# Performance work log

Measured on AMD Instinct MI355X. Metric: run time of the kernel, lower is better.

Reference implementation:

```python
import jax, jax.numpy as jnp
import numpy as np

N_NODES = 50000
N_EDGES = 1_600_000


def add_self_loops(edge_index, n):
    loops = jnp.arange(n, dtype=edge_index.dtype)
    return jnp.concatenate([edge_index, jnp.stack([loops, loops])], axis=1)


def gat_layer(x, edge_index, W, a_src, a_dst, b):
    """PyG GATConv (concat=True, negative_slope=0.2, add_self_loops handled by caller)."""
    src, dst = edge_index[0], edge_index[1]
    n = x.shape[0]
    H, C = a_src.shape
    xp = (x @ W).reshape(n, H, C)                       # [N,H,C] transformed features
    al_src = jnp.einsum('nhc,hc->nh', xp, a_src)        # [N,H]
    al_dst = jnp.einsum('nhc,hc->nh', xp, a_dst)        # [N,H]
    logits = jax.nn.leaky_relu(al_src[src] + al_dst[dst], negative_slope=0.2)  # [E,H]
    m = jax.lax.stop_gradient(jax.ops.segment_max(logits, dst, num_segments=n))
    e = jnp.exp(logits - m[dst])                        # stable segment softmax
    denom = jax.ops.segment_sum(e, dst, num_segments=n)
    alpha = e / denom[dst]                              # [E,H]
    out = jax.ops.segment_sum(xp[src] * alpha[:, :, None], dst, num_segments=n)  # [N,H,C]
    return out.reshape(n, H * C) + b


def setup_inputs() -> dict:
    key = jax.random.key(0)
    ks = jax.random.split(key, 11)
    s = 0.1  # weight scale
    return {
        'x': jax.random.normal(ks[0], (N_NODES, 128), jnp.float32),
        'edge_index': jax.random.randint(ks[1], (2, N_EDGES), 0, N_NODES, jnp.int32),
        'W1': s * jax.random.normal(ks[2], (128, 128), jnp.float32),
        'a_src1': s * jax.random.normal(ks[3], (2, 64), jnp.float32),
        'a_dst1': s * jax.random.normal(ks[4], (2, 64), jnp.float32),
        'b1': s * jax.random.normal(ks[5], (128,), jnp.float32),
        'W2': s * jax.random.normal(ks[6], (128, 64), jnp.float32),
        'a_src2': s * jax.random.normal(ks[7], (2, 32), jnp.float32),
        'a_dst2': s * jax.random.normal(ks[8], (2, 32), jnp.float32),
        'b2': s * jax.random.normal(ks[9], (64,), jnp.float32),
    }


def reference(x, edge_index, W1, a_src1, a_dst1, b1, W2, a_src2, a_dst2, b2):
    ei = add_self_loops(edge_index, x.shape[0])
    encoded = x  # FeatureEncoding with no auxiliary features: identity passthrough
    h = jax.nn.elu(gat_layer(encoded, ei, W1, a_src1, a_dst1, b1))
    out = jax.nn.elu(gat_layer(h, ei, W2, a_src2, a_dst2, b2))
    return (out, encoded)
```

## Files before the change

kernel.cpp:

```cpp
#include <hip/hip_runtime.h>
#include <math.h>

#define N_NODES 50000
#define N_EDGES 1600000
#define EA (N_EDGES + N_NODES)
#define MAXD 128
#define NBUCK 196
#define EPB 4096
#define BCAP 16000

typedef unsigned int uint32;
typedef float f32x4 __attribute__((ext_vector_type(4)));
typedef short s16x8 __attribute__((ext_vector_type(8)));

__device__ inline ushort f2bf(float f) {
  uint32 u = __float_as_uint(f);
  u += 0x7fffu + ((u >> 16) & 1u);
  return (ushort)(u >> 16);
}
__device__ inline float blo(uint32 v) { return __uint_as_float(v << 16); }
__device__ inline float bhi(uint32 v) { return __uint_as_float(v & 0xffff0000u); }
__device__ inline uint32 pack2bf(float a, float b) {
  return (uint32)f2bf(a) | ((uint32)f2bf(b) << 16);
}
__device__ inline int clampi(int v, int lo, int hi) {
  return v < lo ? lo : (v > hi ? hi : v);
}

template<int N, bool ABF>
__global__ __launch_bounds__(256) void gemm_mfma_kernel(
    const void* __restrict__ Ap, const float* __restrict__ B,
    const float* __restrict__ asrc, const float* __restrict__ adst,
    ushort* __restrict__ Cb, float* __restrict__ al, int M) {
  constexpr int KK = 4;
  constexpr int NC = N / 16;
  __shared__ uint32 Bl[KK * NC * 64 * 4];
  const int t = threadIdx.x;

  for (int id = t; id < KK * NC * 64; id += 256) {
    int lane = id & 63;
    int cf = (id >> 6) % NC;
    int kk = (id >> 6) / NC;
    int col = cf * 16 + (lane & 15);
    int k0 = kk * 32 + (lane >> 4) * 8;
    uint32 w0 = pack2bf(B[(k0 + 0) * N + col], B[(k0 + 1) * N + col]);
    uint32 w1 = pack2bf(B[(k0 + 2) * N + col], B[(k0 + 3) * N + col]);
    uint32 w2 = pack2bf(B[(k0 + 4) * N + col], B[(k0 + 5) * N + col]);
    uint32 w3 = pack2bf(B[(k0 + 6) * N + col], B[(k0 + 7) * N + col]);
    *reinterpret_cast<uint4*>(&Bl[id * 4]) = make_uint4(w0, w1, w2, w3);
  }
  __syncthreads();

  const int w = t >> 6, lane = t & 63;
  const int l15 = lane & 15, g4 = lane >> 4;
  const int row0 = blockIdx.x * 64 + w * 16;
  int arow = row0 + l15; if (arow > M - 1) arow = M - 1;
  const int k0 = g4 * 8;

  f32x4 acc[NC];
#pragma unroll
  for (int c = 0; c < NC; ++c) acc[c] = f32x4{0.f, 0.f, 0.f, 0.f};

#pragma unroll
  for (int kk = 0; kk < KK; ++kk) {
    s16x8 af;
    if (ABF) {
      af = *reinterpret_cast<const s16x8*>((const ushort*)Ap + (size_t)arow * 128 + kk * 32 + k0);
    } else {
      const float* A = (const float*)Ap;
      float4 a0 = *reinterpret_cast<const float4*>(A + (size_t)arow * 128 + kk * 32 + k0);
      float4 a1 = *reinterpret_cast<const float4*>(A + (size_t)arow * 128 + kk * 32 + k0 + 4);
      union { uint32 u[4]; s16x8 v; } p;
      p.u[0] = pack2bf(a0.x, a0.y);
      p.u[1] = pack2bf(a0.z, a0.w);
      p.u[2] = pack2bf(a1.x, a1.y);
      p.u[3] = pack2bf(a1.z, a1.w);
      af = p.v;
    }
#pragma unroll
    for (int c = 0; c < NC; ++c) {
      s16x8 bf = *reinterpret_cast<const s16x8*>(&Bl[((kk * NC + c) * 64 + lane) * 4]);
      acc[c] = __builtin_amdgcn_mfma_f32_16x16x32_bf16(af, bf, acc[c], 0, 0, 0);
    }
  }

  float as_c[NC], ad_c[NC];
#pragma unroll
  for (int c = 0; c < NC; ++c) { as_c[c] = asrc[c * 16 + l15]; ad_c[c] = adst[c * 16 + l15]; }
#pragma unroll
  for (int reg = 0; reg < 4; ++reg) {
    int row = row0 + g4 * 4 + reg;
    bool ok = row < M;
    float ps0 = 0.f, ps1 = 0.f, pd0 = 0.f, pd1 = 0.f;
#pragma unroll
    for (int c = 0; c < NC; ++c) {
      float v = acc[c][reg];
      if (ok) Cb[(size_t)row * N + c * 16 + l15] = f2bf(v);
      if (c < NC / 2) { ps0 += v * as_c[c]; pd0 += v * ad_c[c]; }
      else            { ps1 += v * as_c[c]; pd1 += v * ad_c[c]; }
    }
#pragma unroll
    for (int off = 8; off >= 1; off >>= 1) {
      ps0 += __shfl_xor(ps0, off); ps1 += __shfl_xor(ps1, off);
      pd0 += __shfl_xor(pd0, off); pd1 += __shfl_xor(pd1, off);
    }
    if (ok && l15 == 0)
      *reinterpret_cast<float4*>(&al[row * 4]) = make_float4(ps0, ps1, pd0, pd1);
  }
}

__global__ void init_bcur_kernel(int* __restrict__ bcur) {
  int b = blockIdx.x * blockDim.x + threadIdx.x;
  if (b < NBUCK) bcur[b] = b * BCAP;
}

__global__ void partA_kernel(const int* __restrict__ src, const int* __restrict__ dst,
                             int* __restrict__ bcur, uint32* __restrict__ ebuf) {
  __shared__ int h[NBUCK];
  __shared__ int lo[NBUCK + 1];
  __shared__ int rank_[NBUCK];
  __shared__ int gbase[NBUCK];
  __shared__ uint32 staged[EPB];
  const int t = threadIdx.x;
  const int e0 = blockIdx.x * EPB;
  const int ne = min(EPB, N_EDGES - e0);

  for (int i = t; i < NBUCK; i += 256) h[i] = 0;
  __syncthreads();
  for (int i = t; i < ne; i += 256) {
    int d = dst[e0 + i];
    atomicAdd(&h[d >> 8], 1);
  }
  __syncthreads();
  if (t == 0) {
    int a = 0;
    for (int b = 0; b < NBUCK; ++b) { lo[b] = a; a += h[b]; }
    lo[NBUCK] = a;
  }
  __syncthreads();
  for (int i = t; i < NBUCK; i += 256) rank_[i] = lo[i];
  __syncthreads();
  for (int i = t; i < ne; i += 256) {
    int d = dst[e0 + i];
    int s = src[e0 + i];
    int b = d >> 8;
    int r = atomicAdd(&rank_[b], 1);
    staged[r] = ((uint32)s << 8) | (uint32)(d & 255);
  }
  __syncthreads();
  if (t < NBUCK) gbase[t] = atomicAdd(&bcur[t], h[t]);
  __syncthreads();
  for (int i = t; i < ne; i += 256) {
    int a = 0, b = NBUCK;
    while (b - a > 1) { int mid = (a + b) >> 1; if (lo[mid] <= i) a = mid; else b = mid; }
    ebuf[gbase[a] + (i - lo[a])] = staged[i];
  }
}

__global__ void scan196_kernel(const int* __restrict__ bcur, int* __restrict__ bbase,
                               int* __restrict__ row_start) {
  __shared__ int wsh[4];
  const int t = threadIdx.x, lane = t & 63, wv = t >> 6;
  int v = 0;
  if (t < NBUCK) {
    int nn = min(256, N_NODES - t * 256);
    v = (bcur[t] - t * BCAP) + nn;
  }
  int x = v;
  for (int off = 1; off < 64; off <<= 1) {
    int y = __shfl_up(x, off);
    if (lane >= off) x += y;
  }
  if (lane == 63) wsh[wv] = x;
  __syncthreads();
  int wo = 0;
  for (int w = 0; w < wv; ++w) wo += wsh[w];
  if (t < NBUCK) bbase[t] = wo + x - v;
  if (t == 0) row_start[N_NODES] = EA;
}

__global__ __launch_bounds__(256) void partB2_kernel(
    const int* __restrict__ bcur, const int* __restrict__ bbase,
    const uint32* __restrict__ ebuf, int* __restrict__ row_start,
    int* __restrict__ sorted_src) {
  __shared__ uint32 sl[BCAP];
  __shared__ int h[256];
  __shared__ int cur[256];
  __shared__ int wsh[4];
  const int b = blockIdx.x;
  const int t = threadIdx.x, lane = t & 63, wv = t >> 6;
  h[t] = 0;
  __syncthreads();
  const int base = b * BCAP;
  const int len = min(bcur[b] - base, BCAP);
  for (int i = t; i < len; i += 256) {
    uint32 w = ebuf[base + i];
    sl[i] = w;
    atomicAdd(&h[w & 255], 1);
  }
  __syncthreads();
  const int n = b * 256 + t;
  const bool valid = n < N_NODES;
  int v = valid ? h[t] + 1 : 0;
  int x = v;
  for (int off = 1; off < 64; off <<= 1) {
    int y = __shfl_up(x, off);
    if (lane >= off) x += y;
  }
  if (lane == 63) wsh[wv] = x;
  __syncthreads();
  int wo = 0;
  for (int w = 0; w < wv; ++w) wo += wsh[w];
  int rs = bbase[b] + wo + x - v;
  if (valid) {
    row_start[n] = rs;
    sorted_src[rs] = n;
    cur[t] = rs + 1;
  }
  __syncthreads();
  for (int i = t; i < len; i += 256) {
    uint32 w = sl[i];
    int pos = atomicAdd(&cur[w & 255], 1);
    sorted_src[pos] = (int)(w >> 8);
  }
}

template<int HC, bool OUTBF>
__global__ __launch_bounds__(256) void agg_kernel(
    const ushort* __restrict__ xb, const float* __restrict__ al,
    const int* __restrict__ row_start, const int* __restrict__ sorted_src,
    const float* __restrict__ bias, void* __restrict__ outp) {
  __shared__ uint2 pL[4][2][MAXD];
  const int wid = (blockIdx.x * blockDim.x + threadIdx.x) >> 6;
  const int lane = threadIdx.x & 63;
  const int wv = (threadIdx.x >> 6) & 3;
  if (wid >= N_NODES) return;
  const float4* al4 = (const float4*)al;
  const uint32* xb32 = (const uint32*)xb;
  int start = row_start[wid], end = row_start[wid + 1];
  start = clampi(start, 0, EA);
  end   = clampi(end, start, EA);
  const int deg = end - start;
  float4 mya = al4[wid];
  const float ad0 = mya.z, ad1 = mya.w;

  float m0 = -1e30f, m1 = -1e30f, d0 = 0.f, d1 = 0.f;

  if (deg > MAXD) {
    const int c = lane & 31, hh = lane >> 5;
    const int head64 = c >> 4;
    const int head128 = lane >> 5;
    float acc0 = 0.f, acc1 = 0.f;
    for (int i = start + lane; i < end; i += 64) {
      int s = clampi(sorted_src[i], 0, N_NODES - 1);
      float4 a = al4[s];
      float l0 = a.x + ad0; l0 = l0 > 0.f ? l0 : 0.2f * l0;
      float l1 = a.y + ad1; l1 = l1 > 0.f ? l1 : 0.2f * l1;
      m0 = fmaxf(m0, l0); m1 = fmaxf(m1, l1);
    }
    for (int off = 32; off >= 1; off >>= 1) {
      m0 = fmaxf(m0, __shfl_xor(m0, off));
      m1 = fmaxf(m1, __shfl_xor(m1, off));
    }
    for (int i = start + lane; i < end; i += 64) {
      int s = clampi(sorted_src[i], 0, N_NODES - 1);
      float4 a = al4[s];
      float l0 = a.x + ad0; l0 = l0 > 0.f ? l0 : 0.2f * l0;
      float l1 = a.y + ad1; l1 = l1 > 0.f ? l1 : 0.2f * l1;
      d0 += __expf(l0 - m0); d1 += __expf(l1 - m1);
    }
    for (int off = 32; off >= 1; off >>= 1) {
      d0 += __shfl_xor(d0, off);
      d1 += __shfl_xor(d1, off);
    }
    const float inv0 = 1.f / d0, inv1 = 1.f / d1;
    if (HC == 128) {
      const float invh = head128 ? inv1 : inv0;
      const float mh = head128 ? m1 : m0;
      const float adh = head128 ? ad1 : ad0;
      for (int i = start; i < end; ++i) {
        int s = clampi(sorted_src[i], 0, N_NODES - 1);
        float lv = al[s * 4 + head128] + adh;
        lv = lv > 0.f ? lv : 0.2f * lv;
        float a0 = __expf(lv - mh) * invh;
        uint32 v0 = xb32[(size_t)s * 64 + lane];
        acc0 = fmaf(a0, blo(v0), acc0);
        acc1 = fmaf(a0, bhi(v0), acc1);
      }
      float o0 = acc0 + bias[lane * 2];
      float o1 = acc1 + bias[lane * 2 + 1];
      o0 = o0 > 0.f ? o0 : __expf(o0) - 1.f;
      o1 = o1 > 0.f ? o1 : __expf(o1) - 1.f;
      if (OUTBF) ((uint32*)outp)[(size_t)wid * 64 + lane] = pack2bf(o0, o1);
      else *reinterpret_cast<float2*>((float*)outp + (size_t)wid * 128 + lane * 2) = make_float2(o0, o1);
    } else {
      const float invh = head64 ? inv1 : inv0;
      const float mh = head64 ? m1 : m0;
      const float adh = head64 ? ad1 : ad0;
      for (int j = 0; j < deg; j += 2) {
        int jj = j + hh;
        float a0 = 0.f; uint32 v0 = 0;
        if (jj < deg) {
          int s = clampi(sorted_src[start + jj], 0, N_NODES - 1);
          float lv = al[s * 4 + head64] + adh;
          lv = lv > 0.f ? lv : 0.2f * lv;
          a0 = __expf(lv - mh) * invh;
          v0 = xb32[(size_t)s * 32 + c];
        }
        acc0 = fmaf(a0, blo(v0), acc0);
        acc1 = fmaf(a0, bhi(v0), acc1);
      }
      acc0 += __shfl_xor(acc0, 32);
      acc1 += __shfl_xor(acc1, 32);
      if (hh == 0) {
        float o0 = acc0 + bias[c * 2];
        float o1 = acc1 + bias[c * 2 + 1];
        o0 = o0 > 0.f ? o0 : __expf(o0) - 1.f;
        o1 = o1 > 0.f ? o1 : __expf(o1) - 1.f;
        if (OUTBF) ((uint32*)outp)[(size_t)wid * 32 + c] = pack2bf(o0, o1);
        else *reinterpret_cast<float2*>((float*)outp + (size_t)wid * 64 + c * 2) = make_float2(o0, o1);
      }
    }
    return;
  }

  for (int i = start + lane; i < end; i += 64) {
    int s = clampi(sorted_src[i], 0, N_NODES - 1);
    float4 a = al4[s];
    float l0 = a.x + ad0; l0 = l0 > 0.f ? l0 : 0.2f * l0;
    float l1 = a.y + ad1; l1 = l1 > 0.f ? l1 : 0.2f * l1;
    int j = i - start;
    pL[wv][0][j] = make_uint2((uint32)s, __float_as_uint(l0));
    pL[wv][1][j] = make_uint2((uint32)s, __float_as_uint(l1));
    m0 = fmaxf(m0, l0); m1 = fmaxf(m1, l1);
  }
  for (int off = 32; off >= 1; off >>= 1) {
    m0 = fmaxf(m0, __shfl_xor(m0, off));
    m1 = fmaxf(m1, __shfl_xor(m1, off));
  }
  for (int j = lane; j < deg; j += 64) {
    float e0 = __expf(__uint_as_float(pL[wv][0][j].y) - m0);
    float e1 = __expf(__uint_as_float(pL[wv][1][j].y) - m1);
    pL[wv][0][j].y = __float_as_uint(e0);
    pL[wv][1][j].y = __float_as_uint(e1);
    d0 += e0; d1 += e1;
  }
  for (int off = 32; off >= 1; off >>= 1) {
    d0 += __shfl_xor(d0, off);
    d1 += __shfl_xor(d1, off);
  }
  const float inv0 = 1.f / d0, inv1 = 1.f / d1;
  for (int j = lane; j < deg; j += 64) {
    pL[wv][0][j].y = __float_as_uint(__uint_as_float(pL[wv][0][j].y) * inv0);
    pL[wv][1][j].y = __float_as_uint(__uint_as_float(pL[wv][1][j].y) * inv1);
  }

  constexpr int LPR = HC / 8;
  constexpr int EPI = 64 / LPR;
  constexpr int RS  = HC / 2;
  const int q  = lane / LPR;
  const int cc = lane % LPR;
  const int hd = cc / (LPR / 2);
  const uint2* myP = &pL[wv][hd][0];
  const uint32* myx = xb32 + cc * 4;

  float acc[8];
#pragma unroll
  for (int k = 0; k < 8; ++k) acc[k] = 0.f;

  int j = 0;
  for (; j + 2 * EPI <= deg; j += 2 * EPI) {
    uint2 pa = myP[j + q];
    uint2 pb = myP[j + EPI + q];
    const uint4 va = *reinterpret_cast<const uint4*>(myx + (size_t)pa.x * RS);
    const uint4 vb = *reinterpret_cast<const uint4*>(myx + (size_t)pb.x * RS);
    float wa = __uint_as_float(pa.y), wb = __uint_as_float(pb.y);
    acc[0] = fmaf(wa, blo(va.x), acc[0]); acc[1] = fmaf(wa, bhi(va.x), acc[1]);
    acc[2] = fmaf(wa, blo(va.y), acc[2]); acc[3] = fmaf(wa, bhi(va.y), acc[3]);
    acc[4] = fmaf(wa, blo(va.z), acc[4]); acc[5] = fmaf(wa, bhi(va.z), acc[5]);
    acc[6] = fmaf(wa, blo(va.w), acc[6]); acc[7] = fmaf(wa, bhi(va.w), acc[7]);
    acc[0] = fmaf(wb, blo(vb.x), acc[0]); acc[1] = fmaf(wb, bhi(vb.x), acc[1]);
    acc[2] = fmaf(wb, blo(vb.y), acc[2]); acc[3] = fmaf(wb, bhi(vb.y), acc[3]);
    acc[4] = fmaf(wb, blo(vb.z), acc[4]); acc[5] = fmaf(wb, bhi(vb.z), acc[5]);
    acc[6] = fmaf(wb, blo(vb.w), acc[6]); acc[7] = fmaf(wb, bhi(vb.w), acc[7]);
  }
  for (; j < deg; j += EPI) {
    int jj = j + q;
    int jc = jj < deg ? jj : 0;
    uint2 p = myP[jc];
    float w = jj < deg ? __uint_as_float(p.y) : 0.f;
    const uint4 v = *reinterpret_cast<const uint4*>(myx + (size_t)p.x * RS);
    acc[0] = fmaf(w, blo(v.x), acc[0]); acc[1] = fmaf(w, bhi(v.x), acc[1]);
    acc[2] = fmaf(w, blo(v.y), acc[2]); acc[3] = fmaf(w, bhi(v.y), acc[3]);
    acc[4] = fmaf(w, blo(v.z), acc[4]); acc[5] = fmaf(w, bhi(v.z), acc[5]);
    acc[6] = fmaf(w, blo(v.w), acc[6]); acc[7] = fmaf(w, bhi(v.w), acc[7]);
  }

#pragma unroll
  for (int k = 0; k < 8; ++k) {
    if (LPR == 8) acc[k] += __shfl_xor(acc[k], 8);
    acc[k] += __shfl_xor(acc[k], 16);
    acc[k] += __shfl_xor(acc[k], 32);
  }

  if (q == 0) {
    float o[8];
#pragma unroll
    for (int k = 0; k < 8; ++k) {
      float v = acc[k] + bias[cc * 8 + k];
      o[k] = v > 0.f ? v : __expf(v) - 1.f;
    }
    if (OUTBF) {
      uint4 u;
      u.x = pack2bf(o[0], o[1]); u.y = pack2bf(o[2], o[3]);
      u.z = pack2bf(o[4], o[5]); u.w = pack2bf(o[6], o[7]);
      *reinterpret_cast<uint4*>((uint32*)outp + (size_t)wid * RS + cc * 4) = u;
    } else {
      float* op = (float*)outp + (size_t)wid * HC + cc * 8;
      *reinterpret_cast<float4*>(op)     = make_float4(o[0], o[1], o[2], o[3]);
      *reinterpret_cast<float4*>(op + 4) = make_float4(o[4], o[5], o[6], o[7]);
    }
  }
}

__global__ void copy4_kernel(const float4* __restrict__ in, float4* __restrict__ out, int n4) {
  int i = blockIdx.x * blockDim.x + threadIdx.x;
  if (i < n4) out[i] = in[i];
}

extern "C" void kernel_launch(void* const* d_in, const int* in_sizes, int n_in,
                              void* d_out, int out_size, void* d_ws, size_t ws_size,
                              hipStream_t stream) {
  const float* x      = (const float*)d_in[0];
  const int*   ei     = (const int*)d_in[1];
  const float* W1     = (const float*)d_in[2];
  const float* a_src1 = (const float*)d_in[3];
  const float* a_dst1 = (const float*)d_in[4];
  const float* b1     = (const float*)d_in[5];
  const float* W2     = (const float*)d_in[6];
  const float* a_src2 = (const float*)d_in[7];
  const float* a_dst2 = (const float*)d_in[8];
  const float* b2     = (const float*)d_in[9];
  float* out = (float*)d_out;

  char* ws = (char*)d_ws;
  size_t off = 0;
  auto alloc = [&](size_t bytes) {
    void* p = ws + off;
    off = (off + bytes + 255) & ~(size_t)255;
    return p;
  };
  ushort* xb1       = (ushort*)alloc((size_t)N_NODES * 128 * 2);
  ushort* h1b       = (ushort*)alloc((size_t)N_NODES * 128 * 2);
  ushort* xb2       = (ushort*)alloc((size_t)N_NODES * 64 * 2);
  float*  al1       = (float*)alloc((size_t)N_NODES * 4 * 4);
  float*  al2       = (float*)alloc((size_t)N_NODES * 4 * 4);
  int*    row_start = (int*)alloc((size_t)(N_NODES + 1) * 4);
  int*    bbase     = (int*)alloc(256 * 4);
  int*    bcur      = (int*)alloc(NBUCK * 4);
  int*    sorted_src= (int*)alloc((size_t)EA * 4);
  uint32* ebuf      = (uint32*)h1b;

  const int* src = ei;
  const int* dst = ei + N_EDGES;

  const int waveBlocks = (N_NODES * 64) / 256;
  const int partBlocks = (N_EDGES + EPB - 1) / EPB;
  const int gemmBlocks = (N_NODES + 63) / 64;

  init_bcur_kernel<<<1, 256, 0, stream>>>(bcur);
  partA_kernel<<<partBlocks, 256, 0, stream>>>(src, dst, bcur, ebuf);
  scan196_kernel<<<1, 256, 0, stream>>>(bcur, bbase, row_start);
  partB2_kernel<<<NBUCK, 256, 0, stream>>>(bcur, bbase, ebuf, row_start, sorted_src);

  gemm_mfma_kernel<128, false><<<gemmBlocks, 256, 0, stream>>>(x, W1, a_src1, a_dst1, xb1, al1, N_NODES);
  agg_kernel<128, true><<<waveBlocks, 256, 0, stream>>>(xb1, al1, row_start, sorted_src, b1, h1b);

  gemm_mfma_kernel<64, true><<<gemmBlocks, 256, 0, stream>>>(h1b, W2, a_src2, a_dst2, xb2, al2, N_NODES);
  agg_kernel<64, false><<<waveBlocks, 256, 0, stream>>>(xb2, al2, row_start, sorted_src, b2, out);

  copy4_kernel<<<((N_NODES * 128 / 4) + 255) / 256, 256, 0, stream>>>(
      (const float4*)x, (float4*)(out + (size_t)N_NODES * 64), N_NODES * 128 / 4);
}
```

Before: 186.8 us.

## Switch intermediates to fp16 with packed-half aggregation and bucket-tagged scatter

Replaces bf16 storage and MFMA with fp16 (f16 MFMA, pkrtz conversions), and moves the aggregation inner loop to packed half2 multiply-adds with half accumulators. Cross-lane reductions also run on packed halves. The partition kernel now tags each staged edge with its bucket id, so the scatter becomes a direct index instead of a per-element binary search. This cuts ALU work in the gather loop, with a risk of fp16 overflow or precision loss from accumulating in half.

```diff
diff --git a/kernel.cpp b/kernel.cpp
--- a/kernel.cpp
+++ b/kernel.cpp
@@ -11,23 +11,23 @@
 
 typedef unsigned int uint32;
 typedef float f32x4 __attribute__((ext_vector_type(4)));
-typedef short s16x8 __attribute__((ext_vector_type(8)));
-
-__device__ inline ushort f2bf(float f) {
-  uint32 u = __float_as_uint(f);
-  u += 0x7fffu + ((u >> 16) & 1u);
-  return (ushort)(u >> 16);
-}
-__device__ inline float blo(uint32 v) { return __uint_as_float(v << 16); }
-__device__ inline float bhi(uint32 v) { return __uint_as_float(v & 0xffff0000u); }
-__device__ inline uint32 pack2bf(float a, float b) {
-  return (uint32)f2bf(a) | ((uint32)f2bf(b) << 16);
+typedef _Float16 h16x2 __attribute__((ext_vector_type(2)));
+typedef _Float16 f16x8 __attribute__((ext_vector_type(8)));
+
+__device__ inline h16x2 u2h(uint32 u) { return __builtin_bit_cast(h16x2, u); }
+__device__ inline uint32 h2u(h16x2 h) { return __builtin_bit_cast(uint32, h); }
+__device__ inline uint32 pkh(float a, float b) {
+  return __builtin_bit_cast(uint32, __builtin_amdgcn_cvt_pkrtz(a, b));
+}
+__device__ inline ushort f2h(float f) {
+  _Float16 h = (_Float16)f;
+  return __builtin_bit_cast(ushort, h);
 }
 __device__ inline int clampi(int v, int lo, int hi) {
   return v < lo ? lo : (v > hi ? hi : v);
 }
 
-template<int N, bool ABF>
+template<int N, bool AF16>
 __global__ __launch_bounds__(256) void gemm_mfma_kernel(
     const void* __restrict__ Ap, const float* __restrict__ B,
     const float* __restrict__ asrc, const float* __restrict__ adst,
@@ -43,10 +43,10 @@
     int kk = (id >> 6) / NC;
     int col = cf * 16 + (lane & 15);
     int k0 = kk * 32 + (lane >> 4) * 8;
-    uint32 w0 = pack2bf(B[(k0 + 0) * N + col], B[(k0 + 1) * N + col]);
-    uint32 w1 = pack2bf(B[(k0 + 2) * N + col], B[(k0 + 3) * N + col]);
-    uint32 w2 = pack2bf(B[(k0 + 4) * N + col], B[(k0 + 5) * N + col]);
-    uint32 w3 = pack2bf(B[(k0 + 6) * N + col], B[(k0 + 7) * N + col]);
+    uint32 w0 = pkh(B[(k0 + 0) * N + col], B[(k0 + 1) * N + col]);
+    uint32 w1 = pkh(B[(k0 + 2) * N + col], B[(k0 + 3) * N + col]);
+    uint32 w2 = pkh(B[(k0 + 4) * N + col], B[(k0 + 5) * N + col]);
+    uint32 w3 = pkh(B[(k0 + 6) * N + col], B[(k0 + 7) * N + col]);
     *reinterpret_cast<uint4*>(&Bl[id * 4]) = make_uint4(w0, w1, w2, w3);
   }
   __syncthreads();
@@ -63,24 +63,24 @@
 
 #pragma unroll
   for (int kk = 0; kk < KK; ++kk) {
-    s16x8 af;
-    if (ABF) {
-      af = *reinterpret_cast<const s16x8*>((const ushort*)Ap + (size_t)arow * 128 + kk * 32 + k0);
+    f16x8 af;
+    if (AF16) {
+      af = *reinterpret_cast<const f16x8*>((const ushort*)Ap + (size_t)arow * 128 + kk * 32 + k0);
     } else {
       const float* A = (const float*)Ap;
       float4 a0 = *reinterpret_cast<const float4*>(A + (size_t)arow * 128 + kk * 32 + k0);
       float4 a1 = *reinterpret_cast<const float4*>(A + (size_t)arow * 128 + kk * 32 + k0 + 4);
-      union { uint32 u[4]; s16x8 v; } p;
-      p.u[0] = pack2bf(a0.x, a0.y);
-      p.u[1] = pack2bf(a0.z, a0.w);
-      p.u[2] = pack2bf(a1.x, a1.y);
-      p.u[3] = pack2bf(a1.z, a1.w);
+      union { uint32 u[4]; f16x8 v; } p;
+      p.u[0] = pkh(a0.x, a0.y);
+      p.u[1] = pkh(a0.z, a0.w);
+      p.u[2] = pkh(a1.x, a1.y);
+      p.u[3] = pkh(a1.z, a1.w);
       af = p.v;
     }
 #pragma unroll
     for (int c = 0; c < NC; ++c) {
-      s16x8 bf = *reinterpret_cast<const s16x8*>(&Bl[((kk * NC + c) * 64 + lane) * 4]);
-      acc[c] = __builtin_amdgcn_mfma_f32_16x16x32_bf16(af, bf, acc[c], 0, 0, 0);
+      f16x8 bf = *reinterpret_cast<const f16x8*>(&Bl[((kk * NC + c) * 64 + lane) * 4]);
+      acc[c] = __builtin_amdgcn_mfma_f32_16x16x32_f16(af, bf, acc[c], 0, 0, 0);
     }
   }
 
@@ -95,7 +95,7 @@
 #pragma unroll
     for (int c = 0; c < NC; ++c) {
       float v = acc[c][reg];
-      if (ok) Cb[(size_t)row * N + c * 16 + l15] = f2bf(v);
+      if (ok) Cb[(size_t)row * N + c * 16 + l15] = f2h(v);
       if (c < NC / 2) { ps0 += v * as_c[c]; pd0 += v * ad_c[c]; }
       else            { ps1 += v * as_c[c]; pd1 += v * ad_c[c]; }
     }
@@ -117,7 +117,7 @@
 __global__ void partA_kernel(const int* __restrict__ src, const int* __restrict__ dst,
                              int* __restrict__ bcur, uint32* __restrict__ ebuf) {
   __shared__ int h[NBUCK];
-  __shared__ int lo[NBUCK + 1];
+  __shared__ int lo[NBUCK];
   __shared__ int rank_[NBUCK];
   __shared__ int gbase[NBUCK];
   __shared__ uint32 staged[EPB];
@@ -135,7 +135,6 @@
   if (t == 0) {
     int a = 0;
     for (int b = 0; b < NBUCK; ++b) { lo[b] = a; a += h[b]; }
-    lo[NBUCK] = a;
   }
   __syncthreads();
   for (int i = t; i < NBUCK; i += 256) rank_[i] = lo[i];
@@ -145,15 +144,16 @@
     int s = src[e0 + i];
     int b = d >> 8;
     int r = atomicAdd(&rank_[b], 1);
-    staged[r] = ((uint32)s << 8) | (uint32)(d & 255);
+    staged[r] = ((uint32)b << 24) | ((uint32)s << 8) | (uint32)(d & 255);
   }
   __syncthreads();
   if (t < NBUCK) gbase[t] = atomicAdd(&bcur[t], h[t]);
   __syncthreads();
+  if (t < NBUCK) rank_[t] = gbase[t] - lo[t];
+  __syncthreads();
   for (int i = t; i < ne; i += 256) {
-    int a = 0, b = NBUCK;
-    while (b - a > 1) { int mid = (a + b) >> 1; if (lo[mid] <= i) a = mid; else b = mid; }
-    ebuf[gbase[a] + (i - lo[a])] = staged[i];
+    uint32 wd = staged[i];
+    ebuf[rank_[wd >> 24] + i] = wd;
   }
 }
 
@@ -221,13 +221,13 @@
   for (int i = t; i < len; i += 256) {
     uint32 w = sl[i];
     int pos = atomicAdd(&cur[w & 255], 1);
-    sorted_src[pos] = (int)(w >> 8);
-  }
-}
-
-template<int HC, bool OUTBF>
+    sorted_src[pos] = (int)((w >> 8) & 0xffffu);
+  }
+}
+
+template<int HC, bool OUTF16>
 __global__ __launch_bounds__(256) void agg_kernel(
-    const ushort* __restrict__ xb, const float* __restrict__ al,
+    const ushort* __restrict__ xh, const float* __restrict__ al,
     const int* __restrict__ row_start, const int* __restrict__ sorted_src,
     const float* __restrict__ bias, void* __restrict__ outp) {
   __shared__ uint2 pL[4][2][MAXD];
@@ -236,7 +236,7 @@
   const int wv = (threadIdx.x >> 6) & 3;
   if (wid >= N_NODES) return;
   const float4* al4 = (const float4*)al;
-  const uint32* xb32 = (const uint32*)xb;
+  const uint32* xb32 = (const uint32*)xh;
   int start = row_start[wid], end = row_start[wid + 1];
   start = clampi(start, 0, EA);
   end   = clampi(end, start, EA);
@@ -247,10 +247,6 @@
   float m0 = -1e30f, m1 = -1e30f, d0 = 0.f, d1 = 0.f;
 
   if (deg > MAXD) {
-    const int c = lane & 31, hh = lane >> 5;
-    const int head64 = c >> 4;
-    const int head128 = lane >> 5;
-    float acc0 = 0.f, acc1 = 0.f;
     for (int i = start + lane; i < end; i += 64) {
       int s = clampi(sorted_src[i], 0, N_NODES - 1);
       float4 a = al4[s];
@@ -274,52 +270,29 @@
       d1 += __shfl_xor(d1, off);
     }
     const float inv0 = 1.f / d0, inv1 = 1.f / d1;
-    if (HC == 128) {
-      const float invh = head128 ? inv1 : inv0;
-      const float mh = head128 ? m1 : m0;
-      const float adh = head128 ? ad1 : ad0;
+    constexpr int AL = HC / 2;
+    const int cols0 = lane * 2;
+    const int head = cols0 >= HC / 2;
+    const float invh = head ? inv1 : inv0;
+    const float mh = head ? m1 : m0;
+    const float adh = head ? ad1 : ad0;
+    float a0 = 0.f, a1 = 0.f;
+    if (lane < AL) {
       for (int i = start; i < end; ++i) {
         int s = clampi(sorted_src[i], 0, N_NODES - 1);
-        float lv = al[s * 4 + head128] + adh;
+        float lv = al[s * 4 + head] + adh;
         lv = lv > 0.f ? lv : 0.2f * lv;
-        float a0 = __expf(lv - mh) * invh;
-        uint32 v0 = xb32[(size_t)s * 64 + lane];
-        acc0 = fmaf(a0, blo(v0), acc0);
-        acc1 = fmaf(a0, bhi(v0), acc1);
+        float wgt = __expf(lv - mh) * invh;
+        h16x2 hx = u2h(xb32[(size_t)s * AL + lane]);
+        a0 = fmaf(wgt, (float)hx[0], a0);
+        a1 = fmaf(wgt, (float)hx[1], a1);
       }
-      float o0 = acc0 + bias[lane * 2];
-      float o1 = acc1 + bias[lane * 2 + 1];
+      float o0 = a0 + bias[cols0];
+      float o1 = a1 + bias[cols0 + 1];
       o0 = o0 > 0.f ? o0 : __expf(o0) - 1.f;
       o1 = o1 > 0.f ? o1 : __expf(o1) - 1.f;
-      if (OUTBF) ((uint32*)outp)[(size_t)wid * 64 + lane] = pack2bf(o0, o1);
-      else *reinterpret_cast<float2*>((float*)outp + (size_t)wid * 128 + lane * 2) = make_float2(o0, o1);
-    } else {
-      const float invh = head64 ? inv1 : inv0;
-      const float mh = head64 ? m1 : m0;
-      const float adh = head64 ? ad1 : ad0;
-      for (int j = 0; j < deg; j += 2) {
-        int jj = j + hh;
-        float a0 = 0.f; uint32 v0 = 0;
-        if (jj < deg) {
-          int s = clampi(sorted_src[start + jj], 0, N_NODES - 1);
-          float lv = al[s * 4 + head64] + adh;
-          lv = lv > 0.f ? lv : 0.2f * lv;
-          a0 = __expf(lv - mh) * invh;
-          v0 = xb32[(size_t)s * 32 + c];
-        }
-        acc0 = fmaf(a0, blo(v0), acc0);
-        acc1 = fmaf(a0, bhi(v0), acc1);
-      }
-      acc0 += __shfl_xor(acc0, 32);
-      acc1 += __shfl_xor(acc1, 32);
-      if (hh == 0) {
-        float o0 = acc0 + bias[c * 2];
-        float o1 = acc1 + bias[c * 2 + 1];
-        o0 = o0 > 0.f ? o0 : __expf(o0) - 1.f;
-        o1 = o1 > 0.f ? o1 : __expf(o1) - 1.f;
-        if (OUTBF) ((uint32*)outp)[(size_t)wid * 32 + c] = pack2bf(o0, o1);
-        else *reinterpret_cast<float2*>((float*)outp + (size_t)wid * 64 + c * 2) = make_float2(o0, o1);
-      }
+      if (OUTF16) ((uint32*)outp)[(size_t)wid * AL + lane] = pkh(o0, o1);
+      else *reinterpret_cast<float2*>((float*)outp + (size_t)wid * HC + cols0) = make_float2(o0, o1);
     }
     return;
   }
@@ -351,8 +324,10 @@
   }
   const float inv0 = 1.f / d0, inv1 = 1.f / d1;
   for (int j = lane; j < deg; j += 64) {
-    pL[wv][0][j].y = __float_as_uint(__uint_as_float(pL[wv][0][j].y) * inv0);
-    pL[wv][1][j].y = __float_as_uint(__uint_as_float(pL[wv][1][j].y) * inv1);
+    float w0 = __uint_as_float(pL[wv][0][j].y) * inv0;
+    float w1 = __uint_as_float(pL[wv][1][j].y) * inv1;
+    pL[wv][0][j].y = pkh(w0, w0);
+    pL[wv][1][j].y = pkh(w1, w1);
   }
 
   constexpr int LPR = HC / 8;
@@ -364,9 +339,9 @@
   const uint2* myP = &pL[wv][hd][0];
   const uint32* myx = xb32 + cc * 4;
 
-  float acc[8];
-#pragma unroll
-  for (int k = 0; k < 8; ++k) acc[k] = 0.f;
+  h16x2 acc2[4];
+#pragma unroll
+  for (int k = 0; k < 4; ++k) acc2[k] = u2h(0u);
 
   int j = 0;
   for (; j + 2 * EPI <= deg; j += 2 * EPI) {
@@ -374,46 +349,42 @@
     uint2 pb = myP[j + EPI + q];
     const uint4 va = *reinterpret_cast<const uint4*>(myx + (size_t)pa.x * RS);
     const uint4 vb = *reinterpret_cast<const uint4*>(myx + (size_t)pb.x * RS);
-    float wa = __uint_as_float(pa.y), wb = __uint_as_float(pb.y);
-    acc[0] = fmaf(wa, blo(va.x), acc[0]); acc[1] = fmaf(wa, bhi(va.x), acc[1]);
-    acc[2] = fmaf(wa, blo(va.y), acc[2]); acc[3] = fmaf(wa, bhi(va.y), acc[3]);
-    acc[4] = fmaf(wa, blo(va.z), acc[4]); acc[5] = fmaf(wa, bhi(va.z), acc[5]);
-    acc[6] = fmaf(wa, blo(va.w), acc[6]); acc[7] = fmaf(wa, bhi(va.w), acc[7]);
-    acc[0] = fmaf(wb, blo(vb.x), acc[0]); acc[1] = fmaf(wb, bhi(vb.x), acc[1]);
-    acc[2] = fmaf(wb, blo(vb.y), acc[2]); acc[3] = fmaf(wb, bhi(vb.y), acc[3]);
-    acc[4] = fmaf(wb, blo(vb.z), acc[4]); acc[5] = fmaf(wb, bhi(vb.z), acc[5]);
-    acc[6] = fmaf(wb, blo(vb.w), acc[6]); acc[7] = fmaf(wb, bhi(vb.w), acc[7]);
+    h16x2 wa = u2h(pa.y), wb = u2h(pb.y);
+    acc2[0] += wa * u2h(va.x); acc2[1] += wa * u2h(va.y);
+    acc2[2] += wa * u2h(va.z); acc2[3] += wa * u2h(va.w);
+    acc2[0] += wb * u2h(vb.x); acc2[1] += wb * u2h(vb.y);
+    acc2[2] += wb * u2h(vb.z); acc2[3] += wb * u2h(vb.w);
   }
   for (; j < deg; j += EPI) {
     int jj = j + q;
     int jc = jj < deg ? jj : 0;
     uint2 p = myP[jc];
-    float w = jj < deg ? __uint_as_float(p.y) : 0.f;
+    h16x2 w2 = u2h(jj < deg ? p.y : 0u);
     const uint4 v = *reinterpret_cast<const uint4*>(myx + (size_t)p.x * RS);
-    acc[0] = fmaf(w, blo(v.x), acc[0]); acc[1] = fmaf(w, bhi(v.x), acc[1]);
-    acc[2] = fmaf(w, blo(v.y), acc[2]); acc[3] = fmaf(w, bhi(v.y), acc[3]);
-    acc[4] = fmaf(w, blo(v.z), acc[4]); acc[5] = fmaf(w, bhi(v.z), acc[5]);
-    acc[6] = fmaf(w, blo(v.w), acc[6]); acc[7] = fmaf(w, bhi(v.w), acc[7]);
-  }
-
-#pragma unroll
-  for (int k = 0; k < 8; ++k) {
-    if (LPR == 8) acc[k] += __shfl_xor(acc[k], 8);
-    acc[k] += __shfl_xor(acc[k], 16);
-    acc[k] += __shfl_xor(acc[k], 32);
+    acc2[0] += w2 * u2h(v.x); acc2[1] += w2 * u2h(v.y);
+    acc2[2] += w2 * u2h(v.z); acc2[3] += w2 * u2h(v.w);
+  }
+
+#pragma unroll
+  for (int k = 0; k < 4; ++k) {
+    if (LPR == 8) acc2[k] = u2h((uint32)__shfl_xor((int)h2u(acc2[k]), 8)) + acc2[k];
+    acc2[k] = u2h((uint32)__shfl_xor((int)h2u(acc2[k]), 16)) + acc2[k];
+    acc2[k] = u2h((uint32)__shfl_xor((int)h2u(acc2[k]), 32)) + acc2[k];
   }
 
   if (q == 0) {
     float o[8];
 #pragma unroll
-    for (int k = 0; k < 8; ++k) {
-      float v = acc[k] + bias[cc * 8 + k];
-      o[k] = v > 0.f ? v : __expf(v) - 1.f;
-    }
-    if (OUTBF) {
+    for (int k = 0; k < 4; ++k) {
+      o[2 * k]     = (float)acc2[k][0] + bias[cc * 8 + 2 * k];
+      o[2 * k + 1] = (float)acc2[k][1] + bias[cc * 8 + 2 * k + 1];
+    }
+#pragma unroll
+    for (int k = 0; k < 8; ++k) o[k] = o[k] > 0.f ? o[k] : __expf(o[k]) - 1.f;
+    if (OUTF16) {
       uint4 u;
-      u.x = pack2bf(o[0], o[1]); u.y = pack2bf(o[2], o[3]);
-      u.z = pack2bf(o[4], o[5]); u.w = pack2bf(o[6], o[7]);
+      u.x = pkh(o[0], o[1]); u.y = pkh(o[2], o[3]);
+      u.z = pkh(o[4], o[5]); u.w = pkh(o[6], o[7]);
       *reinterpret_cast<uint4*>((uint32*)outp + (size_t)wid * RS + cc * 4) = u;
     } else {
       float* op = (float*)outp + (size_t)wid * HC + cc * 8;
@@ -450,16 +421,16 @@
     off = (off + bytes + 255) & ~(size_t)255;
     return p;
   };
-  ushort* xb1       = (ushort*)alloc((size_t)N_NODES * 128 * 2);
-  ushort* h1b       = (ushort*)alloc((size_t)N_NODES * 128 * 2);
-  ushort* xb2       = (ushort*)alloc((size_t)N_NODES * 64 * 2);
+  ushort* xh1       = (ushort*)alloc((size_t)N_NODES * 128 * 2);
+  ushort* h1h       = (ushort*)alloc((size_t)N_NODES * 128 * 2);
+  ushort* xh2       = (ushort*)alloc((size_t)N_NODES * 64 * 2);
   float*  al1       = (float*)alloc((size_t)N_NODES * 4 * 4);
   float*  al2       = (float*)alloc((size_t)N_NODES * 4 * 4);
   int*    row_start = (int*)alloc((size_t)(N_NODES + 1) * 4);
   int*    bbase     = (int*)alloc(256 * 4);
   int*    bcur      = (int*)alloc(NBUCK * 4);
   int*    sorted_src= (int*)alloc((size_t)EA * 4);
-  uint32* ebuf      = (uint32*)h1b;
+  uint32* ebuf      = (uint32*)h1h;
 
   const int* src = ei;
   const int* dst = ei + N_EDGES;
@@ -473,11 +444,11 @@
   scan196_kernel<<<1, 256, 0, stream>>>(bcur, bbase, row_start);
   partB2_kernel<<<NBUCK, 256, 0, stream>>>(bcur, bbase, ebuf, row_start, sorted_src);
 
-  gemm_mfma_kernel<128, false><<<gemmBlocks, 256, 0, stream>>>(x, W1, a_src1, a_dst1, xb1, al1, N_NODES);
-  agg_kernel<128, true><<<waveBlocks, 256, 0, stream>>>(xb1, al1, row_start, sorted_src, b1, h1b);
-
-  gemm_mfma_kernel<64, true><<<gemmBlocks, 256, 0, stream>>>(h1b, W2, a_src2, a_dst2, xb2, al2, N_NODES);
-  agg_kernel<64, false><<<waveBlocks, 256, 0, stream>>>(xb2, al2, row_start, sorted_src, b2, out);
+  gemm_mfma_kernel<128, false><<<gemmBlocks, 256, 0, stream>>>(x, W1, a_src1, a_dst1, xh1, al1, N_NODES);
+  agg_kernel<128, true><<<waveBlocks, 256, 0, stream>>>(xh1, al1, row_start, sorted_src, b1, h1h);
+
+  gemm_mfma_kernel<64, true><<<gemmBlocks, 256, 0, stream>>>(h1h, W2, a_src2, a_dst2, xh2, al2, N_NODES);
+  agg_kernel<64, false><<<waveBlocks, 256, 0, stream>>>(xh2, al2, row_start, sorted_src, b2, out);
 
   copy4_kernel<<<((N_NODES * 128 / 4) + 255) / 256, 256, 0, stream>>>(
       (const float4*)x, (float4*)(out + (size_t)N_NODES * 64), N_NODES * 128 / 4);
```

Result: faster. 173.7 us (-7.0%).
